# Kernel tuning notes

Measured on AMD Instinct MI355X. Metric: run time of the kernel, lower is better.

The kernel has to match this reference:

```python
import jax, jax.numpy as jnp
import numpy as np

D = 1024
H = 16
DH = D // H

def setup_inputs() -> dict:
    key = jax.random.key(0)
    k1, k2, k3, k4 = jax.random.split(key, 4)
    x = jax.random.normal(k1, (4, 2048, D), dtype=jnp.float32)
    # qkv_linear: Linear(D, D, bias=False); weight stored as (out, in) torch-style
    w_qkv = jax.random.normal(k2, (D, D), dtype=jnp.float32) * (1.0 / np.sqrt(D))
    # final linear: Linear(D, D) with bias
    w_out = jax.random.normal(k3, (D, D), dtype=jnp.float32) * (1.0 / np.sqrt(D))
    b_out = jax.random.normal(k4, (D,), dtype=jnp.float32) * 0.01
    return {"x": x, "w_qkv": w_qkv, "w_out": w_out, "b_out": b_out}

def reference(x, w_qkv, w_out, b_out):
    B, S, E = x.shape
    # Same projection used for Q, K, V (faithful to original module)
    qkv = jnp.einsum('bse,de->bsd', x, w_qkv)           # [B,S,D]
    qkv = qkv.reshape(B, S, H, DH).transpose(0, 2, 1, 3)  # [B,H,S,Dh]
    q = k = v = qkv
    scale = DH ** -0.5
    attn = jnp.einsum('bhqd,bhkd->bhqk', q, k) * scale   # [B,H,S,S]
    attn = jax.nn.softmax(attn, axis=-1)
    out = jnp.einsum('bhqk,bhkd->bhqd', attn, v)         # [B,H,S,Dh]
    out = out.transpose(0, 2, 1, 3).reshape(B, S, E)
    return jnp.einsum('bse,de->bsd', out, w_out) + b_out
```

## Files before the change

### kernel.cpp

```cpp
#include <hip/hip_runtime.h>
#include <hip/hip_bf16.h>
#include <stdint.h>

typedef unsigned short u16;
typedef unsigned int   u32;
typedef unsigned long long u64;
typedef __bf16 bf16x8 __attribute__((ext_vector_type(8)));
typedef float  f32x4  __attribute__((ext_vector_type(4)));
typedef short  s16x4  __attribute__((ext_vector_type(4)));

#define D_MODEL 1024
#define NH 16
#define DHEAD 64
#define BB 4
#define SS 2048
#define MM (BB*SS)

__device__ __forceinline__ u16 f2bf(float f) {
    unsigned int u = __float_as_uint(f);
    u += 0x7fffu + ((u >> 16) & 1u);
    return (u16)(u >> 16);
}
__device__ __forceinline__ float bf2f(u16 s) {
    return __uint_as_float(((unsigned int)s) << 16);
}
__device__ __forceinline__ u32 pkbf(float a, float b) {
    __hip_bfloat162 h = __float22bfloat162_rn(make_float2(a, b));
    return *(u32*)&h;
}

union U8 {
    uint4 q;
    u16   v[8];
    bf16x8 f;
};
union P4 {
    u32   u[2];
    s16x4 h;
};

#define N4X (MM * D_MODEL / 4)
#define N4W (D_MODEL * D_MODEL / 4)
__global__ __launch_bounds__(256) void cvt_all_kernel(const float* __restrict__ x,
                                                      const float* __restrict__ wq,
                                                      const float* __restrict__ wo,
                                                      u16* __restrict__ xb,
                                                      u16* __restrict__ wqb,
                                                      u16* __restrict__ wob) {
    int i = blockIdx.x * 256 + threadIdx.x;
    const float* s; u16* d; int off;
    if (i < N4X)            { s = x;  d = xb;  off = i; }
    else if (i < N4X + N4W) { s = wq; d = wqb; off = i - N4X; }
    else                    { s = wo; d = wob; off = i - N4X - N4W; }
    float4 f = ((const float4*)s)[off];
    u32 o[2] = { pkbf(f.x, f.y), pkbf(f.z, f.w) };
    ((uint2*)d)[off] = *(const uint2*)o;
}

template <bool PERMUTE_OUT>
__device__ __forceinline__ void gemm_body(const u16* __restrict__ A,
                                          const u16* __restrict__ Bt,
                                          const float* __restrict__ Bo,
                                          u16* __restrict__ Cq, u16* __restrict__ CqT,
                                          float* __restrict__ Out)
{
    __shared__ __align__(16) u16 As[128*64];
    __shared__ __align__(16) u16 Bs[128*64];

    const int tid  = threadIdx.x;
    const int wave = tid >> 6;
    const int lane = tid & 63;
    const int quad = lane >> 4;
    const int l16  = lane & 15;
    const int bm = blockIdx.x >> 3;
    const int bn = blockIdx.x & 7;
    const int wm = wave >> 1, wn = wave & 1;

    f32x4 acc[4][4] = {};

    const int rp = tid >> 3;
    const int ch = tid & 7;
    const int sc = ch ^ (rp & 7);

    const u16* Ab = A  + (size_t)(bm * 128 + rp) * D_MODEL + sc * 8;
    const u16* Bb = Bt + (size_t)(bn * 128 + rp) * D_MODEL + sc * 8;
    const int xr = l16 & 7;

    for (int k0 = 0; k0 < D_MODEL; k0 += 64) {
#pragma unroll
        for (int p = 0; p < 4; ++p) {
            __builtin_amdgcn_global_load_lds(
                (__attribute__((address_space(1))) void*)(Ab + (size_t)(32*p) * D_MODEL + k0),
                (__attribute__((address_space(3))) void*)(As + p*2048 + tid*8), 16, 0, 0);
            __builtin_amdgcn_global_load_lds(
                (__attribute__((address_space(1))) void*)(Bb + (size_t)(32*p) * D_MODEL + k0),
                (__attribute__((address_space(3))) void*)(Bs + p*2048 + tid*8), 16, 0, 0);
        }
        __syncthreads();

#pragma unroll
        for (int ks = 0; ks < 2; ++ks) {
            bf16x8 af[4], bfr[4];
#pragma unroll
            for (int t = 0; t < 4; ++t)
                af[t] = *(const bf16x8*)(const void*)(
                    As + (wm*64 + t*16 + l16)*64 + (((ks*4 + quad) ^ xr) * 8));
#pragma unroll
            for (int t = 0; t < 4; ++t)
                bfr[t] = *(const bf16x8*)(const void*)(
                    Bs + (wn*64 + t*16 + l16)*64 + (((ks*4 + quad) ^ xr) * 8));
#pragma unroll
            for (int i = 0; i < 4; ++i)
#pragma unroll
                for (int j = 0; j < 4; ++j)
                    acc[i][j] = __builtin_amdgcn_mfma_f32_16x16x32_bf16(af[i], bfr[j], acc[i][j], 0, 0, 0);
        }
        __syncthreads();
    }

    const int rowbase = bm*128 + wm*64;
    const int colbase = bn*128 + wn*64;
    if (PERMUTE_OUT) {
#pragma unroll
        for (int j = 0; j < 4; ++j) {
            const int col = colbase + j*16 + l16;
            const int h = col >> 6, dh = col & 63;
#pragma unroll
            for (int i = 0; i < 4; ++i) {
                const int row0 = rowbase + i*16 + quad*4;
                const int b = row0 >> 11, s0 = row0 & (SS - 1);
#pragma unroll
                for (int r = 0; r < 4; ++r)
                    Cq[(((size_t)(b*NH + h))*SS + s0 + r)*DHEAD + dh] = f2bf(acc[i][j][r]);
                u64 w = (u64)pkbf(acc[i][j][0], acc[i][j][1])
                      | ((u64)pkbf(acc[i][j][2], acc[i][j][3]) << 32);
                *(u64*)(CqT + ((size_t)((b*NH + h)*DHEAD + dh))*SS + s0) = w;
            }
        }
    } else {
#pragma unroll
        for (int j = 0; j < 4; ++j) {
            const int col = colbase + j*16 + l16;
            const float bias = Bo[col];
#pragma unroll
            for (int i = 0; i < 4; ++i) {
#pragma unroll
                for (int r = 0; r < 4; ++r) {
                    const int row = rowbase + i*16 + quad*4 + r;
                    Out[(size_t)row * D_MODEL + col] = acc[i][j][r] + bias;
                }
            }
        }
    }
}

__global__ __launch_bounds__(256) void gemm_qkv_kernel(const u16* __restrict__ A,
                                                       const u16* __restrict__ Bt,
                                                       u16* __restrict__ Cq,
                                                       u16* __restrict__ CqT) {
    gemm_body<true>(A, Bt, nullptr, Cq, CqT, nullptr);
}

__global__ __launch_bounds__(256) void gemm_out_kernel(const u16* __restrict__ A,
                                                       const u16* __restrict__ Bt,
                                                       const float* __restrict__ Bo,
                                                       float* __restrict__ Out) {
    gemm_body<false>(A, Bt, Bo, nullptr, nullptr, Out);
}

__global__ __launch_bounds__(256, 4) void attn_kernel(const u16* __restrict__ qkv,
                                                      const u16* __restrict__ qkvT,
                                                      u16* __restrict__ outb)
{
    __shared__ __align__(16) u16 Ks[2*2048];
    __shared__ __align__(16) u16 Vt[2*2048];

    const int tid  = threadIdx.x;
    const int wave = tid >> 6;
    const int lane = tid & 63;
    const int quad = lane >> 4;
    const int l16  = lane & 15;

    const int bh   = blockIdx.x >> 4;
    const int qblk = blockIdx.x & 15;
    const int b = bh >> 4, h = bh & 15;
    const int qbase = qblk * 128 + wave * 32;

    const u16* Qp = qkv + (size_t)bh * SS * DHEAD;
    const float qscale = 0.125f * 1.4426950408889634f;

    bf16x8 qb[2][2];
#pragma unroll
    for (int nt = 0; nt < 2; ++nt)
#pragma unroll
        for (int ks = 0; ks < 2; ++ks) {
            U8 raw; raw.q = *(const uint4*)(Qp + (size_t)(qbase + nt*16 + l16)*DHEAD + ks*32 + quad*8);
            U8 w;
#pragma unroll
            for (int jj = 0; jj < 4; ++jj)
                ((u32*)&w)[jj] = pkbf(bf2f(raw.v[2*jj]) * qscale, bf2f(raw.v[2*jj+1]) * qscale);
            qb[nt][ks] = w.f;
        }

    const int rK = tid >> 3, cK = (tid & 7) ^ ((rK >> 1) & 7);
    const u16* srcK = qkv  + (size_t)bh * SS * DHEAD + rK * DHEAD + cK * 8;
    const int rV = tid >> 2, cV = (tid & 3) ^ ((rV >> 1) & 3);
    const u16* srcV = qkvT + (size_t)bh * DHEAD * SS + (size_t)rV * SS + cV * 8;

    const int h8 = (l16 >> 1) & 7, h4 = (l16 >> 1) & 3;
    const int ko0 = l16*64 + ((quad)     ^ h8) * 8;
    const int ko1 = l16*64 + ((4 + quad) ^ h8) * 8;
    const int vo0 = l16*32 + (((quad >> 1))     ^ h4) * 8 + (quad & 1) * 4;
    const int vo1 = l16*32 + ((2 + (quad >> 1)) ^ h4) * 8 + (quad & 1) * 4;

    f32x4 ot[4][2] = {};
    float lacc[2]  = {0.0f, 0.0f};

    __builtin_amdgcn_global_load_lds(
        (__attribute__((address_space(1))) void*)(srcK),
        (__attribute__((address_space(3))) void*)(Ks + tid*8), 16, 0, 0);
    __builtin_amdgcn_global_load_lds(
        (__attribute__((address_space(1))) void*)(srcV),
        (__attribute__((address_space(3))) void*)(Vt + tid*8), 16, 0, 0);

#pragma unroll 2
    for (int kt = 0; kt < SS/32; ++kt) {
        __syncthreads();
        if (kt < SS/32 - 1) {
            __builtin_amdgcn_global_load_lds(
                (__attribute__((address_space(1))) void*)(srcK + (size_t)(kt+1)*32*DHEAD),
                (__attribute__((address_space(3))) void*)(Ks + ((kt+1)&1)*2048 + tid*8), 16, 0, 0);
            __builtin_amdgcn_global_load_lds(
                (__attribute__((address_space(1))) void*)(srcV + (kt+1)*32),
                (__attribute__((address_space(3))) void*)(Vt + ((kt+1)&1)*2048 + tid*8), 16, 0, 0);
        }
        const u16* Kb = Ks + (kt&1)*2048;
        const u16* Vb = Vt + (kt&1)*2048;

        s16x4 vfr[4][2];
#pragma unroll
        for (int dt = 0; dt < 4; ++dt) {
            vfr[dt][0] = *(const s16x4*)(const void*)(Vb + dt*512 + vo0);
            vfr[dt][1] = *(const s16x4*)(const void*)(Vb + dt*512 + vo1);
        }

        s16x4 pf[2][2];
#pragma unroll
        for (int mt = 0; mt < 2; ++mt) {
            f32x4 s[2] = {};
            bf16x8 kf0 = *(const bf16x8*)(const void*)(Kb + mt*1024 + ko0);
            bf16x8 kf1 = *(const bf16x8*)(const void*)(Kb + mt*1024 + ko1);
            __builtin_amdgcn_s_setprio(1);
#pragma unroll
            for (int nt = 0; nt < 2; ++nt)
                s[nt] = __builtin_amdgcn_mfma_f32_16x16x32_bf16(kf0, qb[nt][0], s[nt], 0, 0, 0);
#pragma unroll
            for (int nt = 0; nt < 2; ++nt)
                s[nt] = __builtin_amdgcn_mfma_f32_16x16x32_bf16(kf1, qb[nt][1], s[nt], 0, 0, 0);
            __builtin_amdgcn_s_setprio(0);
#pragma unroll
            for (int nt = 0; nt < 2; ++nt) {
                float p0 = __builtin_amdgcn_exp2f(s[nt][0]);
                float p1 = __builtin_amdgcn_exp2f(s[nt][1]);
                float p2 = __builtin_amdgcn_exp2f(s[nt][2]);
                float p3 = __builtin_amdgcn_exp2f(s[nt][3]);
                lacc[nt] += (p0 + p1) + (p2 + p3);
                P4 pk_; pk_.u[0] = pkbf(p0, p1); pk_.u[1] = pkbf(p2, p3);
                pf[mt][nt] = pk_.h;
            }
        }

        __builtin_amdgcn_s_setprio(1);
#pragma unroll
        for (int dt = 0; dt < 4; ++dt)
#pragma unroll
            for (int mt = 0; mt < 2; ++mt) {
                ot[dt][0] = __builtin_amdgcn_mfma_f32_16x16x16bf16_1k(vfr[dt][mt], pf[mt][0], ot[dt][0], 0, 0, 0);
                ot[dt][1] = __builtin_amdgcn_mfma_f32_16x16x16bf16_1k(vfr[dt][mt], pf[mt][1], ot[dt][1], 0, 0, 0);
            }
        __builtin_amdgcn_s_setprio(0);
    }

    float inv[2];
#pragma unroll
    for (int nt = 0; nt < 2; ++nt) {
        float v = lacc[nt];
        v += __shfl_xor(v, 16, 64);
        v += __shfl_xor(v, 32, 64);
        inv[nt] = 1.0f / v;
    }

#pragma unroll
    for (int dt = 0; dt < 4; ++dt)
#pragma unroll
        for (int nt = 0; nt < 2; ++nt) {
            u64 w = (u64)pkbf(ot[dt][nt][0]*inv[nt], ot[dt][nt][1]*inv[nt])
                  | ((u64)pkbf(ot[dt][nt][2]*inv[nt], ot[dt][nt][3]*inv[nt]) << 32);
            *(u64*)(outb + ((size_t)(b*SS + qbase + nt*16 + l16))*D_MODEL
                         + h*64 + dt*16 + quad*4) = w;
        }
}

extern "C" void kernel_launch(void* const* d_in, const int* in_sizes, int n_in,
                              void* d_out, int out_size, void* d_ws, size_t ws_size,
                              hipStream_t stream)
{
    (void)in_sizes; (void)n_in; (void)out_size; (void)ws_size;
    const float* x  = (const float*)d_in[0];
    const float* wq = (const float*)d_in[1];
    const float* wo = (const float*)d_in[2];
    const float* bo = (const float*)d_in[3];

    char* ws = (char*)d_ws;
    u16* xb    = (u16*)(ws);
    u16* wqb   = (u16*)(ws + (size_t)(16 << 20));
    u16* wob   = (u16*)(ws + (size_t)(18 << 20));
    u16* qkvb  = (u16*)(ws + (size_t)(20 << 20));
    u16* qkvTb = (u16*)(ws + (size_t)(36 << 20));
    u16* attb  = xb;

    cvt_all_kernel<<<(N4X + 2*N4W) / 256, 256, 0, stream>>>(x, wq, wo, xb, wqb, wob);
    gemm_qkv_kernel<<<(MM/128) * (D_MODEL/128), 256, 0, stream>>>(xb, wqb, qkvb, qkvTb);
    attn_kernel<<<BB * NH * (SS/128), 256, 0, stream>>>(qkvb, qkvTb, attb);
    gemm_out_kernel<<<(MM/128) * (D_MODEL/128), 256, 0, stream>>>(attb, wob, bo, (float*)d_out);
}
```

Baseline: 239.6 us.

## Use 16x16x32 MFMA for PV and swizzle block order for cache locality

The P·V product now concatenates the two 16-key sub-tiles into one 8-wide bf16 operand. It issues half as many 16x16x32 MFMAs in place of pairs of 16x16x16 ones, and computes both S sub-tiles before exponentiating. Block indices in the GEMM and attention kernels are remapped so groups of eight consecutive blocks share the same column tile or query block across different row tiles or heads, aiming for better L2 reuse. The risk is higher register pressure from holding both S tiles at once. The k-ordering of the concatenated operands must also match between V and P.

```diff
diff --git a/kernel.cpp b/kernel.cpp
--- a/kernel.cpp
+++ b/kernel.cpp
@@ -34,10 +34,8 @@
     u16   v[8];
     bf16x8 f;
 };
-union P4 {
-    u32   u[2];
-    s16x4 h;
-};
+union B8 { u32 w[4]; bf16x8 f; };
+union V8 { s16x4 h[2]; bf16x8 f; };
 
 #define N4X (MM * D_MODEL / 4)
 #define N4W (D_MODEL * D_MODEL / 4)
@@ -72,8 +70,10 @@
     const int lane = tid & 63;
     const int quad = lane >> 4;
     const int l16  = lane & 15;
-    const int bm = blockIdx.x >> 3;
-    const int bn = blockIdx.x & 7;
+    const int dsw = blockIdx.x;
+    const int sl  = dsw >> 3;
+    const int bm  = ((sl >> 3) << 3) + (dsw & 7);
+    const int bn  = sl & 7;
     const int wm = wave >> 1, wn = wave & 1;
 
     f32x4 acc[4][4] = {};
@@ -181,8 +181,10 @@
     const int quad = lane >> 4;
     const int l16  = lane & 15;
 
-    const int bh   = blockIdx.x >> 4;
-    const int qblk = blockIdx.x & 15;
+    const int dsw  = blockIdx.x;
+    const int sl   = dsw >> 3;
+    const int bh   = ((sl >> 4) << 3) + (dsw & 7);
+    const int qblk = sl & 15;
     const int b = bh >> 4, h = bh & 15;
     const int qbase = qblk * 128 + wave * 32;
 
@@ -237,47 +239,52 @@
         const u16* Kb = Ks + (kt&1)*2048;
         const u16* Vb = Vt + (kt&1)*2048;
 
-        s16x4 vfr[4][2];
+        V8 vt[4];
 #pragma unroll
         for (int dt = 0; dt < 4; ++dt) {
-            vfr[dt][0] = *(const s16x4*)(const void*)(Vb + dt*512 + vo0);
-            vfr[dt][1] = *(const s16x4*)(const void*)(Vb + dt*512 + vo1);
-        }
-
-        s16x4 pf[2][2];
+            vt[dt].h[0] = *(const s16x4*)(const void*)(Vb + dt*512 + vo0);
+            vt[dt].h[1] = *(const s16x4*)(const void*)(Vb + dt*512 + vo1);
+        }
+
+        f32x4 s[2][2] = {};
+        __builtin_amdgcn_s_setprio(1);
 #pragma unroll
         for (int mt = 0; mt < 2; ++mt) {
-            f32x4 s[2] = {};
             bf16x8 kf0 = *(const bf16x8*)(const void*)(Kb + mt*1024 + ko0);
             bf16x8 kf1 = *(const bf16x8*)(const void*)(Kb + mt*1024 + ko1);
-            __builtin_amdgcn_s_setprio(1);
 #pragma unroll
             for (int nt = 0; nt < 2; ++nt)
-                s[nt] = __builtin_amdgcn_mfma_f32_16x16x32_bf16(kf0, qb[nt][0], s[nt], 0, 0, 0);
+                s[mt][nt] = __builtin_amdgcn_mfma_f32_16x16x32_bf16(kf0, qb[nt][0], s[mt][nt], 0, 0, 0);
 #pragma unroll
             for (int nt = 0; nt < 2; ++nt)
-                s[nt] = __builtin_amdgcn_mfma_f32_16x16x32_bf16(kf1, qb[nt][1], s[nt], 0, 0, 0);
-            __builtin_amdgcn_s_setprio(0);
-#pragma unroll
-            for (int nt = 0; nt < 2; ++nt) {
-                float p0 = __builtin_amdgcn_exp2f(s[nt][0]);
-                float p1 = __builtin_amdgcn_exp2f(s[nt][1]);
-                float p2 = __builtin_amdgcn_exp2f(s[nt][2]);
-                float p3 = __builtin_amdgcn_exp2f(s[nt][3]);
-                lacc[nt] += (p0 + p1) + (p2 + p3);
-                P4 pk_; pk_.u[0] = pkbf(p0, p1); pk_.u[1] = pkbf(p2, p3);
-                pf[mt][nt] = pk_.h;
-            }
+                s[mt][nt] = __builtin_amdgcn_mfma_f32_16x16x32_bf16(kf1, qb[nt][1], s[mt][nt], 0, 0, 0);
+        }
+        __builtin_amdgcn_s_setprio(0);
+
+        bf16x8 pb[2];
+#pragma unroll
+        for (int nt = 0; nt < 2; ++nt) {
+            float p00 = __builtin_amdgcn_exp2f(s[0][nt][0]);
+            float p01 = __builtin_amdgcn_exp2f(s[0][nt][1]);
+            float p02 = __builtin_amdgcn_exp2f(s[0][nt][2]);
+            float p03 = __builtin_amdgcn_exp2f(s[0][nt][3]);
+            float p10 = __builtin_amdgcn_exp2f(s[1][nt][0]);
+            float p11 = __builtin_amdgcn_exp2f(s[1][nt][1]);
+            float p12 = __builtin_amdgcn_exp2f(s[1][nt][2]);
+            float p13 = __builtin_amdgcn_exp2f(s[1][nt][3]);
+            lacc[nt] += ((p00 + p01) + (p02 + p03)) + ((p10 + p11) + (p12 + p13));
+            B8 t;
+            t.w[0] = pkbf(p00, p01); t.w[1] = pkbf(p02, p03);
+            t.w[2] = pkbf(p10, p11); t.w[3] = pkbf(p12, p13);
+            pb[nt] = t.f;
         }
 
         __builtin_amdgcn_s_setprio(1);
 #pragma unroll
-        for (int dt = 0; dt < 4; ++dt)
-#pragma unroll
-            for (int mt = 0; mt < 2; ++mt) {
-                ot[dt][0] = __builtin_amdgcn_mfma_f32_16x16x16bf16_1k(vfr[dt][mt], pf[mt][0], ot[dt][0], 0, 0, 0);
-                ot[dt][1] = __builtin_amdgcn_mfma_f32_16x16x16bf16_1k(vfr[dt][mt], pf[mt][1], ot[dt][1], 0, 0, 0);
-            }
+        for (int dt = 0; dt < 4; ++dt) {
+            ot[dt][0] = __builtin_amdgcn_mfma_f32_16x16x32_bf16(vt[dt].f, pb[0], ot[dt][0], 0, 0, 0);
+            ot[dt][1] = __builtin_amdgcn_mfma_f32_16x16x32_bf16(vt[dt].f, pb[1], ot[dt][1], 0, 0, 0);
+        }
         __builtin_amdgcn_s_setprio(0);
     }
 
```

After: 227.5 us. 5.1% less time.
